# Kernel optimization log

Measured on AMD Instinct MI355X. Metric: run time of the kernel, lower is better.

Reference implementation:

```python
import jax, jax.numpy as jnp
import numpy as np

# Fixed graph/model dims (see shape_source)
C = 16      # cardinality
SUB = 64    # representation_size // cardinality
R = 1024    # representation_size
E = 1024    # node_encoding_size
S = 1024    # processed spatial feature size
G = 256     # global (FPN) channels
NH = 64     # number of human nodes
N = 256     # total number of nodes (humans first)
P = NH * N  # number of (human, node) pairs
EPS = 1e-5


def _layernorm(x, g, b):
    mu = jnp.mean(x, axis=-1, keepdims=True)
    var = jnp.var(x, axis=-1, keepdims=True)
    return (x - mu) * jax.lax.rsqrt(var + EPS) * g + b


def _pair_head(app, spat, W1, b1, W2, b2, W3, b3):
    # app: [P_or_1, A], spat: [P, S] -> [P, R]  (sum over cardinality; NO outer relu)
    a1 = jnp.einsum('pi,cis->cps', app, W1) + b1[:, None, :]   # [C,P_or_1,SUB]
    a2 = jnp.einsum('pj,cjs->cps', spat, W2) + b2[:, None, :]  # [C,P,SUB]
    h = jax.nn.relu(a1 * a2)                                   # broadcast over P
    return jnp.einsum('cps,csr->pr', h, W3) + jnp.sum(b3, axis=0)


def reference(node_encodings, spatial_raw, global_feat,
              sp_W1, sp_b1, sp_W2, sp_b2, sp_W3, sp_b3,
              ah_W1, ah_b1, ah_W2, ah_b2, ah_W3, ah_b3,
              o2s_W1, o2s_b1, o2s_W2, o2s_b2, o2s_W3, o2s_b3,
              s2o_W1, s2o_b1, s2o_W2, s2o_b2, s2o_W3, s2o_b3,
              ahg_W1, ahg_b1, ahg_W2, ahg_b2, ahg_W3, ahg_b3,
              adj_W, adj_b, lnh_g, lnh_b, lno_g, lno_b):
    # spatial head MLP: 36 -> 128 -> 256 -> 1024 with ReLU
    sp = jax.nn.relu(spatial_raw @ sp_W1 + sp_b1)
    sp = jax.nn.relu(sp @ sp_W2 + sp_b2)
    sp = jax.nn.relu(sp @ sp_W3 + sp_b3)            # [P, S]
    sp3 = sp.reshape(NH, N, S)                      # [NH, N, S]

    x_idx = jnp.repeat(jnp.arange(NH), N)           # [P]
    y_idx = jnp.tile(jnp.arange(N), NH)             # [P]

    h_enc = node_encodings[:NH]                     # humans are permuted to the top
    o_enc = node_encodings

    for _ in range(1):  # num_iter
        app_pairs = jnp.concatenate([h_enc[x_idx], o_enc[y_idx]], axis=1)  # [P, 2E]
        weights = jax.nn.relu(_pair_head(app_pairs, sp, ah_W1, ah_b1, ah_W2, ah_b2, ah_W3, ah_b3))
        adj = (weights @ adj_W + adj_b).reshape(NH, N)

        # obj_to_sub (node_type='object'): appearance = all node encodings
        a1 = jnp.einsum('ni,cis->cns', o_enc, o2s_W1) + o2s_b1[:, None, :]          # [C,N,SUB]
        a2 = jnp.einsum('hnj,cjs->chns', sp3, o2s_W2) + o2s_b2[:, None, None, :]    # [C,NH,N,SUB]
        m = jnp.einsum('chns,csr->hnr', jax.nn.relu(a1[:, None] * a2), o2s_W3) + jnp.sum(o2s_b3, axis=0)
        msg_h = jax.nn.relu(jnp.sum(jax.nn.softmax(adj, axis=1)[..., None] * m, axis=1))  # [NH,R]
        h_enc = _layernorm(h_enc + msg_h, lnh_g, lnh_b)

        # sub_to_obj (node_type='human'): appearance = human encodings
        a1 = jnp.einsum('hi,cis->chs', h_enc, s2o_W1) + s2o_b1[:, None, :]          # [C,NH,SUB]
        a2 = jnp.einsum('hnj,cjs->cnhs', sp3, s2o_W2) + s2o_b2[:, None, None, :]    # [C,N,NH,SUB]
        m = jnp.einsum('cnhs,csr->nhr', jax.nn.relu(a1[:, None] * a2), s2o_W3) + jnp.sum(s2o_b3, axis=0)
        msg_o = jax.nn.relu(jnp.sum(jax.nn.softmax(adj.T, axis=1)[..., None] * m, axis=1))  # [N,R]
        o_enc = _layernorm(o_enc + msg_o, lno_g, lno_b)

    app_final = jnp.concatenate([h_enc[x_idx], o_enc[y_idx]], axis=1)               # [P, 2E]
    f_local = jax.nn.relu(_pair_head(app_final, sp, ah_W1, ah_b1, ah_W2, ah_b2, ah_W3, ah_b3))
    f_glob = jax.nn.relu(_pair_head(global_feat, sp, ahg_W1, ahg_b1, ahg_W2, ahg_b2, ahg_W3, ahg_b3))
    return jnp.concatenate([f_local, f_glob], axis=1)  # [P, 2R]


def setup_inputs() -> dict:
    key = jax.random.key(0)
    ks = iter(jax.random.split(key, 64))
    def rn(shape, scale=0.05):
        return jax.random.normal(next(ks), shape, dtype=jnp.float32) * scale
    inp = {
        'node_encodings': jax.random.normal(next(ks), (N, E), dtype=jnp.float32),
        'spatial_raw': jax.random.normal(next(ks), (P, 36), dtype=jnp.float32),
        'global_feat': jax.random.normal(next(ks), (1, G), dtype=jnp.float32),
        'sp_W1': rn((36, 128)), 'sp_b1': jnp.zeros(128, jnp.float32),
        'sp_W2': rn((128, 256)), 'sp_b2': jnp.zeros(256, jnp.float32),
        'sp_W3': rn((256, S)), 'sp_b3': jnp.zeros(S, jnp.float32),
        'ah_W1': rn((C, 2 * E, SUB)), 'ah_b1': jnp.zeros((C, SUB), jnp.float32),
        'ah_W2': rn((C, S, SUB)), 'ah_b2': jnp.zeros((C, SUB), jnp.float32),
        'ah_W3': rn((C, SUB, R)), 'ah_b3': jnp.zeros((C, R), jnp.float32),
        'o2s_W1': rn((C, E, SUB)), 'o2s_b1': jnp.zeros((C, SUB), jnp.float32),
        'o2s_W2': rn((C, S, SUB)), 'o2s_b2': jnp.zeros((C, SUB), jnp.float32),
        'o2s_W3': rn((C, SUB, R)), 'o2s_b3': jnp.zeros((C, R), jnp.float32),
        's2o_W1': rn((C, E, SUB)), 's2o_b1': jnp.zeros((C, SUB), jnp.float32),
        's2o_W2': rn((C, S, SUB)), 's2o_b2': jnp.zeros((C, SUB), jnp.float32),
        's2o_W3': rn((C, SUB, R)), 's2o_b3': jnp.zeros((C, R), jnp.float32),
        'ahg_W1': rn((C, G, SUB)), 'ahg_b1': jnp.zeros((C, SUB), jnp.float32),
        'ahg_W2': rn((C, S, SUB)), 'ahg_b2': jnp.zeros((C, SUB), jnp.float32),
        'ahg_W3': rn((C, SUB, R)), 'ahg_b3': jnp.zeros((C, R), jnp.float32),
        'adj_W': rn((R, 1)), 'adj_b': jnp.zeros(1, jnp.float32),
        'lnh_g': jnp.ones(E, jnp.float32), 'lnh_b': jnp.zeros(E, jnp.float32),
        'lno_g': jnp.ones(E, jnp.float32), 'lno_b': jnp.zeros(E, jnp.float32),
    }
    return inp
```

## Files before the change

### kernel.cpp

```cpp
#include <hip/hip_runtime.h>
#include <hip/hip_bf16.h>
#include <stdint.h>
#include <stddef.h>

using bf16 = __hip_bfloat16;
typedef __bf16 bf16x8 __attribute__((ext_vector_type(8)));
typedef float f32x4 __attribute__((ext_vector_type(4)));

#define P_  16384

__device__ __forceinline__ void gload16(const void* g, void* l) {
    __builtin_amdgcn_global_load_lds((const __attribute__((address_space(1))) void*)g,
                                     (__attribute__((address_space(3))) void*)l, 16, 0, 0);
}

struct GArgs {
    const bf16* A; const bf16* B; void* C;
    const float* bias;
    const float* aux1;
    int M, N, K, ldc, kchunk;
    void* dst1; void* dst2; void* dst3; void* dstH;
    const float* cb0; const float* cb1; const float* cb2; const float* cb3;
    const float* a1gv; const float* Ahp; const float* Aop; const float* b1p;
};

template<int MODE, bool RELU, bool BIAS>
__global__ __launch_bounds__(256, 4)
void gemm_bt(GArgs g)
{
    __shared__ __align__(16) bf16 As[128 * 64];
    __shared__ __align__(16) bf16 Bs[128 * 64];

    const int tid  = threadIdx.x;
    const int wave = tid >> 6;
    const int lane = tid & 63;
    const int tileM = blockIdx.x * 128;
    const int tileN = blockIdx.y * 128;
    const int wr = (wave >> 1) << 6;
    const int wc = (wave & 1) << 6;
    const int M = g.M, N = g.N, K = g.K;

    const bf16* Ap = g.A; const bf16* Bp = g.B;
    void* Cp = g.C; const float* biasp = g.bias;
    if (MODE == 0 && blockIdx.z == 1) {
        Ap = (const bf16*)g.dst1; Bp = (const bf16*)g.dst2;
        Cp = g.dst3; biasp = g.cb1;
    }

    f32x4 acc[4][4] = {};

    const int gk = (((lane & 7) ^ (lane >> 3)) << 3);
    int arow[4], brow[4];
    #pragma unroll
    for (int j = 0; j < 4; ++j) {
        int r = wave * 32 + j * 8 + (lane >> 3);
        int gr = tileM + r; if (gr > M - 1) gr = M - 1; arow[j] = gr;
        int gn = tileN + r; if (gn > N - 1) gn = N - 1; brow[j] = gn;
    }
    const int m0 = wr + (lane & 15);
    const int n0 = wc + (lane & 15);
    const int q  = lane >> 4;

    int kbeg = 0, kend = K;
    if constexpr (MODE == 2) { kbeg = blockIdx.z * 64; kend = kbeg + 64; }

    for (int k0 = kbeg; k0 < kend; k0 += 64) {
        #pragma unroll
        for (int j = 0; j < 4; ++j) {
            int c = wave * 256 + j * 64 + lane;
            gload16(Ap + (size_t)arow[j] * K + k0 + gk, (void*)(As + c * 8));
            gload16(Bp + (size_t)brow[j] * K + k0 + gk, (void*)(Bs + c * 8));
        }
        __syncthreads();
        #pragma unroll
        for (int kk = 0; kk < 2; ++kk) {
            const int gs = ((kk << 2) + q) ^ (lane & 7);
            bf16x8 af[4], bfv[4];
            #pragma unroll
            for (int i = 0; i < 4; ++i) {
                af[i]  = *(const bf16x8*)(As + (m0 + i * 16) * 64 + gs * 8);
                bfv[i] = *(const bf16x8*)(Bs + (n0 + i * 16) * 64 + gs * 8);
            }
            #pragma unroll
            for (int i = 0; i < 4; ++i)
                #pragma unroll
                for (int j = 0; j < 4; ++j)
                    acc[i][j] = __builtin_amdgcn_mfma_f32_16x16x32_bf16(af[i], bfv[j], acc[i][j], 0, 0, 0);
        }
        __syncthreads();
    }

    const int rbase = tileM + wr + ((lane >> 4) << 2);
    const int cbase = tileN + wc + (lane & 15);

    if constexpr (MODE == 0 || MODE == 1) {
        #pragma unroll
        for (int i = 0; i < 4; ++i)
            #pragma unroll
            for (int j = 0; j < 4; ++j)
                #pragma unroll
                for (int r = 0; r < 4; ++r) {
                    int grow = rbase + i * 16 + r;
                    if (grow >= M) continue;
                    int gcol = cbase + j * 16;
                    float v = acc[i][j][r];
                    if (BIAS) v += biasp[gcol];
                    if (RELU) v = fmaxf(v, 0.f);
                    if (MODE == 1) ((bf16*)Cp)[(size_t)grow * g.ldc + gcol] = __float2bfloat16(v);
                    else           ((float*)Cp)[(size_t)grow * g.ldc + gcol] = v;
                }
    } else if constexpr (MODE == 2) {
        #pragma unroll
        for (int i = 0; i < 4; ++i)
            #pragma unroll
            for (int j = 0; j < 4; ++j)
                #pragma unroll
                for (int r = 0; r < 4; ++r) {
                    int grow = rbase + i * 16 + r;
                    if (grow >= M) continue;
                    atomicAdd((float*)Cp + (size_t)grow * g.ldc + cbase + j * 16, acc[i][j][r]);
                }
    } else if constexpr (MODE == 6) {
        #pragma unroll
        for (int i = 0; i < 4; ++i)
            #pragma unroll
            for (int r = 0; r < 4; ++r) {
                float s = 0.f;
                #pragma unroll
                for (int j = 0; j < 4; ++j) {
                    int gcol = cbase + j * 16;
                    s += fmaxf(acc[i][j][r] + biasp[gcol], 0.f) * g.aux1[gcol];
                }
                s += __shfl_xor(s, 1); s += __shfl_xor(s, 2);
                s += __shfl_xor(s, 4); s += __shfl_xor(s, 8);
                if ((lane & 15) == 0)
                    atomicAdd((float*)Cp + rbase + i * 16 + r, s);
            }
    } else if constexpr (MODE == 9) {
        int grp = tileN >> 10;
        int lcb = (tileN & 1023) + wc + (lane & 15);
        #pragma unroll
        for (int i = 0; i < 4; ++i)
            #pragma unroll
            for (int j = 0; j < 4; ++j)
                #pragma unroll
                for (int r = 0; r < 4; ++r) {
                    int p    = rbase + i * 16 + r;
                    int lcol = lcb + j * 16;
                    float accv = acc[i][j][r];
                    if (grp == 0) {
                        bf16 a2b = __float2bfloat16(accv + g.cb0[lcol]);
                        ((bf16*)Cp)[(size_t)p * 1024 + lcol] = a2b;
                        float a1 = g.Ahp[((size_t)(p >> 8)) * 3072 + lcol]
                                 + g.Aop[((size_t)(p & 255)) * 3072 + lcol] + g.b1p[lcol];
                        ((bf16*)g.dstH)[(size_t)p * 1024 + lcol] =
                            __float2bfloat16(fmaxf(a1 * (float)a2b, 0.f));
                    } else if (grp == 1) {
                        ((bf16*)g.dst1)[(size_t)p * 1024 + lcol] =
                            __float2bfloat16(accv + g.cb1[lcol]);
                    } else if (grp == 2) {
                        ((bf16*)g.dst2)[(size_t)p * 1024 + lcol] =
                            __float2bfloat16(accv + g.cb2[lcol]);
                    } else {
                        float a2v = accv + g.cb3[lcol];
                        ((bf16*)g.dst3)[(size_t)p * 1024 + lcol] =
                            __float2bfloat16(fmaxf(g.a1gv[lcol] * a2v, 0.f));
                    }
                }
    }
}

static GArgs mkargs(const bf16* A, const bf16* B, void* C, const float* bias,
                    const float* aux1, int M, int N, int K, int ldc, int kchunk)
{
    GArgs g{};
    g.A = A; g.B = B; g.C = C; g.bias = bias; g.aux1 = aux1;
    g.M = M; g.N = N; g.K = K; g.ldc = ldc; g.kchunk = kchunk;
    return g;
}

__global__ void reduce_o2s(const bf16* __restrict__ a2, const float* __restrict__ a1,
                           const float* __restrict__ b1, const float* __restrict__ sh,
                           bf16* __restrict__ out)
{
    int h = blockIdx.y, cq = blockIdx.x;
    int ng = threadIdx.x >> 5, ct = threadIdx.x & 31;
    int c = cq * 256 + ct * 8;
    float b1v[8], accv[8] = {};
    #pragma unroll
    for (int j = 0; j < 8; ++j) b1v[j] = b1[c + j];
    const float* shh = sh + h * 256;
    for (int n = ng; n < 256; n += 8) {
        float w = shh[n];
        bf16x8 a2v = *(const bf16x8*)(a2 + ((size_t)(h * 256 + n) << 10) + c);
        const float* a1p = a1 + (size_t)n * 3072 + c;
        #pragma unroll
        for (int j = 0; j < 8; ++j)
            accv[j] += w * fmaxf((a1p[j] + b1v[j]) * (float)a2v[j], 0.f);
    }
    __shared__ float red[8][264];
    #pragma unroll
    for (int j = 0; j < 8; ++j) red[ng][ct * 8 + j] = accv[j];
    __syncthreads();
    for (int s = 4; s > 0; s >>= 1) {
        if (ng < s)
            #pragma unroll
            for (int j = 0; j < 8; ++j) red[ng][ct * 8 + j] += red[ng + s][ct * 8 + j];
        __syncthreads();
    }
    if (ng == 0) {
        bf16x8 o;
        #pragma unroll
        for (int j = 0; j < 8; ++j) o[j] = (__bf16)red[0][ct * 8 + j];
        *(bf16x8*)(out + (size_t)h * 1024 + c) = o;
    }
}

__global__ void reduce_s2o(const bf16* __restrict__ a2, const float* __restrict__ a1,
                           const float* __restrict__ b1, const float* __restrict__ so,
                           bf16* __restrict__ out)
{
    int n = blockIdx.y, cq = blockIdx.x;
    int hg = threadIdx.x >> 5, ct = threadIdx.x & 31;
    int c = cq * 256 + ct * 8;
    float b1v[8], accv[8] = {};
    #pragma unroll
    for (int j = 0; j < 8; ++j) b1v[j] = b1[c + j];
    const float* son = so + n * 64;
    #pragma unroll
    for (int hh = 0; hh < 8; ++hh) {
        int h = hg + hh * 8;
        float w = son[h];
        bf16x8 a2v = *(const bf16x8*)(a2 + ((size_t)(h * 256 + n) << 10) + c);
        const float* a1p = a1 + (size_t)h * 2048 + c;
        #pragma unroll
        for (int j = 0; j < 8; ++j)
            accv[j] += w * fmaxf((a1p[j] + b1v[j]) * (float)a2v[j], 0.f);
    }
    __shared__ float red[8][264];
    #pragma unroll
    for (int j = 0; j < 8; ++j) red[hg][ct * 8 + j] = accv[j];
    __syncthreads();
    for (int s = 4; s > 0; s >>= 1) {
        if (hg < s)
            #pragma unroll
            for (int j = 0; j < 8; ++j) red[hg][ct * 8 + j] += red[hg + s][ct * 8 + j];
        __syncthreads();
    }
    if (hg == 0) {
        bf16x8 o;
        #pragma unroll
        for (int j = 0; j < 8; ++j) o[j] = (__bf16)red[0][ct * 8 + j];
        *(bf16x8*)(out + (size_t)n * 1024 + c) = o;
    }
}

__global__ void transp(const float* __restrict__ src, bf16* __restrict__ dst,
                       int rows, int cols, size_t sstride, size_t dstride)
{
    const float* s = src + blockIdx.z * sstride;
    bf16*        d = dst + blockIdx.z * dstride;
    __shared__ float tile[32][33];
    int c0 = blockIdx.x * 32, r0 = blockIdx.y * 32;
    int x = threadIdx.x, y = threadIdx.y;
    for (int yy = y; yy < 32; yy += 8) {
        int r = r0 + yy, c = c0 + x;
        tile[yy][x] = (r < rows && c < cols) ? s[(size_t)r * cols + c] : 0.f;
    }
    __syncthreads();
    for (int yy = y; yy < 32; yy += 8) {
        int c = c0 + yy, r = r0 + x;
        if (c < cols && r < rows) d[(size_t)c * rows + r] = __float2bfloat16(tile[x][yy]);
    }
}

struct T9 { const float* s[9]; bf16* d[9]; size_t ss[9]; };
__global__ void transp64b(T9 t)
{
    int pair = blockIdx.z >> 4, slice = blockIdx.z & 15;
    const float* s = t.s[pair] + slice * t.ss[pair];
    bf16*        d = t.d[pair] + slice * 65536;
    __shared__ float tile[32][33];
    int c0 = blockIdx.x * 32, r0 = blockIdx.y * 32;
    int x = threadIdx.x, y = threadIdx.y;
    for (int yy = y; yy < 32; yy += 8)
        tile[yy][x] = s[(size_t)(r0 + yy) * 64 + c0 + x];
    __syncthreads();
    for (int yy = y; yy < 32; yy += 8)
        d[(size_t)(c0 + yy) * 1024 + r0 + x] = __float2bfloat16(tile[x][yy]);
}

struct T4 { const float* s[4]; bf16* d[4]; };
__global__ void transp1024b(T4 t)
{
    const float* s = t.s[blockIdx.z];
    bf16*        d = t.d[blockIdx.z];
    __shared__ float tile[32][33];
    int c0 = blockIdx.x * 32, r0 = blockIdx.y * 32;
    int x = threadIdx.x, y = threadIdx.y;
    for (int yy = y; yy < 32; yy += 8)
        tile[yy][x] = s[(size_t)(r0 + yy) * 1024 + c0 + x];
    __syncthreads();
    for (int yy = y; yy < 32; yy += 8)
        d[(size_t)(c0 + yy) * 1024 + r0 + x] = __float2bfloat16(tile[x][yy]);
}

__global__ void conv_spw1(const float* __restrict__ src, bf16* __restrict__ dst) {
    int i = blockIdx.x * 256 + threadIdx.x;
    if (i >= 128 * 64) return;
    int k = i & 63, n = i >> 6;
    dst[i] = __float2bfloat16(k < 36 ? src[k * 128 + n] : 0.f);
}

__global__ void pad_spatial(const float* __restrict__ src, bf16* __restrict__ dst) {
    int i = blockIdx.x * 256 + threadIdx.x;
    int k = i & 63, p = i >> 6;
    dst[i] = __float2bfloat16(k < 36 ? src[p * 36 + k] : 0.f);
}

__global__ void cast_f2b(const float* __restrict__ src, bf16* __restrict__ dst, int n) {
    int i = blockIdx.x * 256 + threadIdx.x;
    if (i < n) dst[i] = __float2bfloat16(src[i]);
}

struct S4 { const float* s[4]; float* d[4]; };
__global__ void sumb3b(S4 a) {
    int i = blockIdx.x * 256 + threadIdx.x;
    int pair = i >> 10, r = i & 1023;
    const float* b3 = a.s[pair];
    float s = 0.f;
    #pragma unroll
    for (int c = 0; c < 16; ++c) s += b3[c * 1024 + r];
    a.d[pair][r] = s;
}

__global__ void hbuild(const float* __restrict__ Ah, int ah_ld,
                       const float* __restrict__ Ao, int ao_ld,
                       const float* __restrict__ b1, const bf16* __restrict__ a2,
                       bf16* __restrict__ H)
{
    size_t base = ((size_t)blockIdx.x * 256 + threadIdx.x) * 8;
    int cs = (int)(base & 1023);
    int p  = (int)(base >> 10);
    const float* ph = Ah + (size_t)(p >> 8) * ah_ld + cs;
    const float* po = Ao + (size_t)(p & 255) * ao_ld + cs;
    bf16x8 av = *(const bf16x8*)(a2 + base);
    bf16x8 o;
    #pragma unroll
    for (int j = 0; j < 8; ++j) {
        float a1 = ph[j] + po[j] + b1[cs + j];
        o[j] = (__bf16)fmaxf(a1 * (float)av[j], 0.f);
    }
    *(bf16x8*)(H + base) = o;
}

__global__ void softmax_h(const float* __restrict__ adj, float* __restrict__ sh) {
    int h = blockIdx.x, n = threadIdx.x;
    __shared__ float red[256];
    float v = adj[h * 256 + n];
    red[n] = v; __syncthreads();
    for (int s = 128; s > 0; s >>= 1) { if (n < s) red[n] = fmaxf(red[n], red[n + s]); __syncthreads(); }
    float m = red[0]; __syncthreads();
    float e = expf(v - m);
    red[n] = e; __syncthreads();
    for (int s = 128; s > 0; s >>= 1) { if (n < s) red[n] += red[n + s]; __syncthreads(); }
    sh[h * 256 + n] = e / red[0];
}

__global__ void softmax_o(const float* __restrict__ adj, float* __restrict__ so) {
    int n = blockIdx.x, h = threadIdx.x;
    float v = adj[h * 256 + n];
    float m = v;
    #pragma unroll
    for (int off = 32; off; off >>= 1) m = fmaxf(m, __shfl_xor(m, off));
    float e = expf(v - m);
    float s = e;
    #pragma unroll
    for (int off = 32; off; off >>= 1) s += __shfl_xor(s, off);
    so[n * 64 + h] = e / s;
}

__global__ void ln_k(const float* __restrict__ x, const float* __restrict__ msgraw,
                     const float* __restrict__ sb3,
                     const float* __restrict__ g, const float* __restrict__ bb,
                     bf16* __restrict__ out)
{
    int row = blockIdx.x, t = threadIdx.x;
    const float* xr = x + (size_t)row * 1024;
    const float* mr = msgraw + (size_t)row * 1024;
    float v[4]; float s = 0.f, ss = 0.f;
    #pragma unroll
    for (int j = 0; j < 4; ++j) {
        int i = t + j * 256;
        v[j] = xr[i] + fmaxf(mr[i] + sb3[i], 0.f);
        s += v[j]; ss += v[j] * v[j];
    }
    __shared__ float r1[256], r2[256];
    r1[t] = s; r2[t] = ss; __syncthreads();
    for (int k = 128; k > 0; k >>= 1) { if (t < k) { r1[t] += r1[t + k]; r2[t] += r2[t + k]; } __syncthreads(); }
    float mean = r1[0] * (1.f / 1024.f);
    float var  = r2[0] * (1.f / 1024.f) - mean * mean;
    float inv  = rsqrtf(var + 1e-5f);
    #pragma unroll
    for (int j = 0; j < 4; ++j) {
        int i = t + j * 256;
        out[(size_t)row * 1024 + i] = __float2bfloat16((v[j] - mean) * inv * g[i] + bb[i]);
    }
}

__global__ void a1g_k(const float* __restrict__ gf, const float* __restrict__ W1,
                      const float* __restrict__ b1, float* __restrict__ a1g)
{
    int cs = blockIdx.x * 256 + threadIdx.x;
    int c = cs >> 6, s = cs & 63;
    float acc = b1[cs];
    for (int g = 0; g < 256; ++g) acc += gf[g] * W1[((size_t)c * 256 + g) * 64 + s];
    a1g[cs] = acc;
}

extern "C" void kernel_launch(void* const* d_in, const int* in_sizes, int n_in,
                              void* d_out, int out_size, void* d_ws, size_t ws_size,
                              hipStream_t stream)
{
    const float* node_enc = (const float*)d_in[0];
    const float* spatial  = (const float*)d_in[1];
    const float* gfeat    = (const float*)d_in[2];
    const float* sp_W1 = (const float*)d_in[3];  const float* sp_b1 = (const float*)d_in[4];
    const float* sp_W2 = (const float*)d_in[5];  const float* sp_b2 = (const float*)d_in[6];
    const float* sp_W3 = (const float*)d_in[7];  const float* sp_b3 = (const float*)d_in[8];
    const float* ah_W1 = (const float*)d_in[9];  const float* ah_b1 = (const float*)d_in[10];
    const float* ah_W2 = (const float*)d_in[11]; const float* ah_b2 = (const float*)d_in[12];
    const float* ah_W3 = (const float*)d_in[13]; const float* ah_b3 = (const float*)d_in[14];
    const float* o2s_W1 = (const float*)d_in[15]; const float* o2s_b1 = (const float*)d_in[16];
    const float* o2s_W2 = (const float*)d_in[17]; const float* o2s_b2 = (const float*)d_in[18];
    const float* o2s_W3 = (const float*)d_in[19]; const float* o2s_b3 = (const float*)d_in[20];
    const float* s2o_W1 = (const float*)d_in[21]; const float* s2o_b1 = (const float*)d_in[22];
    const float* s2o_W2 = (const float*)d_in[23]; const float* s2o_b2 = (const float*)d_in[24];
    const float* s2o_W3 = (const float*)d_in[25]; const float* s2o_b3 = (const float*)d_in[26];
    const float* ahg_W1 = (const float*)d_in[27]; const float* ahg_b1 = (const float*)d_in[28];
    const float* ahg_W2 = (const float*)d_in[29]; const float* ahg_b2 = (const float*)d_in[30];
    const float* ahg_W3 = (const float*)d_in[31]; const float* ahg_b3 = (const float*)d_in[32];
    const float* adj_W = (const float*)d_in[33];
    const float* lnh_g = (const float*)d_in[35]; const float* lnh_b = (const float*)d_in[36];
    const float* lno_g = (const float*)d_in[37]; const float* lno_b = (const float*)d_in[38];

    char* w = (char*)d_ws;
    auto alloc = [&](size_t bytes) { char* p = w; w += (bytes + 255) & ~(size_t)255; return p; };
    bf16*  sp      = (bf16*)alloc((size_t)P_ * 1024 * 2);
    bf16*  a2_ah   = (bf16*)alloc((size_t)P_ * 1024 * 2);
    bf16*  Hbuf    = (bf16*)alloc((size_t)P_ * 1024 * 2);
    bf16*  a2_o2s  = (bf16*)alloc((size_t)P_ * 1024 * 2);
    bf16*  a2_s2o  = (bf16*)alloc((size_t)P_ * 1024 * 2);
    bf16*  H_ahg   = (bf16*)alloc((size_t)P_ * 1024 * 2);
    bf16*  spat_pad= (bf16*)alloc((size_t)P_ * 64 * 2);
    bf16*  spL1    = (bf16*)alloc((size_t)P_ * 128 * 2);
    bf16*  spL2    = (bf16*)alloc((size_t)P_ * 256 * 2);
    bf16*  enc_bf  = (bf16*)alloc(256 * 1024 * 2);
    bf16*  henc_bf = (bf16*)alloc(64 * 1024 * 2);
    bf16*  oenc_bf = (bf16*)alloc(256 * 1024 * 2);
    bf16*  HredH   = (bf16*)alloc(64 * 1024 * 2);
    bf16*  HredO   = (bf16*)alloc(256 * 1024 * 2);
    bf16*  spW1t   = (bf16*)alloc(128 * 64 * 2);
    bf16*  spW2t   = (bf16*)alloc(256 * 128 * 2);
    bf16*  spW3t   = (bf16*)alloc(1024 * 256 * 2);
    bf16*  W2cat   = (bf16*)alloc((size_t)4096 * 1024 * 2);
    bf16*  W1cat3  = (bf16*)alloc((size_t)3072 * 1024 * 2);
    bf16*  W1catF  = (bf16*)alloc((size_t)2048 * 1024 * 2);
    bf16*  ahW3t   = (bf16*)alloc(1024 * 1024 * 2);
    bf16*  o2sW3t  = (bf16*)alloc(1024 * 1024 * 2);
    bf16*  s2oW3t  = (bf16*)alloc(1024 * 1024 * 2);
    bf16*  ahgW3t  = (bf16*)alloc(1024 * 1024 * 2);
    float* Aoa1x = (float*)alloc(256 * 3072 * 4);
    float* A1f   = (float*)alloc(64 * 2048 * 4);
    float* Ao_f  = (float*)alloc(256 * 1024 * 4);
    size_t z1_bytes = (size_t)(256 * 3072 + 64 * 2048 + 256 * 1024) * 4 + 1024;
    float* adjv  = (float*)alloc(P_ * 4);
    float* msgh  = (float*)alloc(64 * 1024 * 4);
    float* msgo  = (float*)alloc(256 * 1024 * 4);
    size_t z2_bytes = (size_t)(P_ + 64 * 1024 + 256 * 1024) * 4 + 1024;
    float* sh    = (float*)alloc(P_ * 4);
    float* so    = (float*)alloc(P_ * 4);
    float* a1g   = (float*)alloc(1024 * 4);
    float* sb3_ah  = (float*)alloc(4096);
    float* sb3_o2s = (float*)alloc(4096);
    float* sb3_s2o = (float*)alloc(4096);
    float* sb3_ahg = (float*)alloc(4096);

    hipMemsetAsync(Aoa1x, 0, z1_bytes, stream);
    hipMemsetAsync(adjv,  0, z2_bytes, stream);

    {
        T9 t;
        t.s[0] = ah_W1;                     t.d[0] = W1cat3 + (size_t)2048 * 1024; t.ss[0] = (size_t)2048 * 64;
        t.s[1] = ah_W1 + (size_t)1024 * 64; t.d[1] = W1cat3;                       t.ss[1] = (size_t)2048 * 64;
        t.s[2] = o2s_W1;                    t.d[2] = W1cat3 + (size_t)1024 * 1024; t.ss[2] = 65536;
        t.s[3] = s2o_W1;                    t.d[3] = W1catF;                       t.ss[3] = 65536;
        t.s[4] = ah_W1;                     t.d[4] = W1catF + (size_t)1024 * 1024; t.ss[4] = (size_t)2048 * 64;
        t.s[5] = ah_W2;                     t.d[5] = W2cat;                        t.ss[5] = 65536;
        t.s[6] = o2s_W2;                    t.d[6] = W2cat + (size_t)1024 * 1024;  t.ss[6] = 65536;
        t.s[7] = s2o_W2;                    t.d[7] = W2cat + (size_t)2048 * 1024;  t.ss[7] = 65536;
        t.s[8] = ahg_W2;                    t.d[8] = W2cat + (size_t)3072 * 1024;  t.ss[8] = 65536;
        transp64b<<<dim3(2, 32, 144), dim3(32, 8), 0, stream>>>(t);
    }
    {
        T4 t;
        t.s[0] = ah_W3;  t.d[0] = ahW3t;
        t.s[1] = o2s_W3; t.d[1] = o2sW3t;
        t.s[2] = s2o_W3; t.d[2] = s2oW3t;
        t.s[3] = ahg_W3; t.d[3] = ahgW3t;
        transp1024b<<<dim3(32, 32, 4), dim3(32, 8), 0, stream>>>(t);
    }
    dim3 tb(32, 8);
    conv_spw1<<<32, 256, 0, stream>>>(sp_W1, spW1t);
    transp<<<dim3(8, 4, 1),  tb, 0, stream>>>(sp_W2, spW2t, 128, 256, 0, 0);
    transp<<<dim3(32, 8, 1), tb, 0, stream>>>(sp_W3, spW3t, 256, 1024, 0, 0);
    pad_spatial<<<4096, 256, 0, stream>>>(spatial, spat_pad);
    cast_f2b<<<1024, 256, 0, stream>>>(node_enc, enc_bf, 256 * 1024);
    {
        S4 a;
        a.s[0] = ah_b3;  a.d[0] = sb3_ah;
        a.s[1] = o2s_b3; a.d[1] = sb3_o2s;
        a.s[2] = s2o_b3; a.d[2] = sb3_s2o;
        a.s[3] = ahg_b3; a.d[3] = sb3_ahg;
        sumb3b<<<16, 256, 0, stream>>>(a);
    }
    a1g_k<<<4, 256, 0, stream>>>(gfeat, ahg_W1, ahg_b1, a1g);

    gemm_bt<2, false, false><<<dim3(2, 24, 16), 256, 0, stream>>>(
        mkargs(enc_bf, W1cat3, Aoa1x, nullptr, nullptr, 256, 3072, 1024, 3072, 64));

    gemm_bt<1, true, true><<<dim3(128, 1), 256, 0, stream>>>(
        mkargs(spat_pad, spW1t, spL1, sp_b1, nullptr, P_, 128, 64, 128, 0));
    gemm_bt<1, true, true><<<dim3(128, 2), 256, 0, stream>>>(
        mkargs(spL1, spW2t, spL2, sp_b2, nullptr, P_, 256, 128, 256, 0));
    gemm_bt<1, true, true><<<dim3(128, 8), 256, 0, stream>>>(
        mkargs(spL2, spW3t, sp, sp_b3, nullptr, P_, 1024, 256, 1024, 0));

    {
        GArgs g = mkargs(sp, W2cat, a2_ah, nullptr, nullptr, P_, 4096, 1024, 1024, 0);
        g.dst1 = a2_o2s; g.dst2 = a2_s2o; g.dst3 = H_ahg; g.dstH = Hbuf;
        g.cb0 = ah_b2; g.cb1 = o2s_b2; g.cb2 = s2o_b2; g.cb3 = ahg_b2;
        g.a1gv = a1g; g.Ahp = Aoa1x + 2048; g.Aop = Aoa1x; g.b1p = ah_b1;
        gemm_bt<9, false, false><<<dim3(128, 32), 256, 0, stream>>>(g);
    }

    gemm_bt<6, false, false><<<dim3(128, 8), 256, 0, stream>>>(
        mkargs(Hbuf, ahW3t, adjv, sb3_ah, adj_W, P_, 1024, 1024, 1024, 0));
    softmax_h<<<64, 256, 0, stream>>>(adjv, sh);
    softmax_o<<<256, 64, 0, stream>>>(adjv, so);

    reduce_o2s<<<dim3(4, 64), 256, 0, stream>>>(a2_o2s, Aoa1x + 1024, o2s_b1, sh, HredH);
    gemm_bt<2, false, false><<<dim3(1, 8, 16), 256, 0, stream>>>(
        mkargs(HredH, o2sW3t, msgh, nullptr, nullptr, 64, 1024, 1024, 1024, 64));
    ln_k<<<64, 256, 0, stream>>>(node_enc, msgh, sb3_o2s, lnh_g, lnh_b, henc_bf);

    gemm_bt<2, false, false><<<dim3(1, 16, 16), 256, 0, stream>>>(
        mkargs(henc_bf, W1catF, A1f, nullptr, nullptr, 64, 2048, 1024, 2048, 64));

    reduce_s2o<<<dim3(4, 256), 256, 0, stream>>>(a2_s2o, A1f, s2o_b1, so, HredO);
    gemm_bt<2, false, false><<<dim3(2, 8, 16), 256, 0, stream>>>(
        mkargs(HredO, s2oW3t, msgo, nullptr, nullptr, 256, 1024, 1024, 1024, 64));
    ln_k<<<256, 256, 0, stream>>>(node_enc, msgo, sb3_s2o, lno_g, lno_b, oenc_bf);

    gemm_bt<2, false, false><<<dim3(2, 8, 16), 256, 0, stream>>>(
        mkargs(oenc_bf, W1cat3, Ao_f, nullptr, nullptr, 256, 1024, 1024, 1024, 64));
    hbuild<<<8192, 256, 0, stream>>>(A1f + 1024, 2048, Ao_f, 1024, ah_b1, a2_ah, Hbuf);

    {
        GArgs g = mkargs(Hbuf, ahW3t, (float*)d_out, sb3_ah, nullptr, P_, 1024, 1024, 2048, 0);
        g.dst1 = (void*)H_ahg; g.dst2 = (void*)ahgW3t;
        g.dst3 = (void*)((float*)d_out + 1024); g.cb1 = sb3_ahg;
        gemm_bt<0, true, true><<<dim3(128, 8, 2), 256, 0, stream>>>(g);
    }

    (void)in_sizes; (void)n_in; (void)out_size; (void)ws_size;
}
```

Baseline: 798.2 us.

## Add 256x256 double-buffered GEMM kernel for large pair GEMMs

Introduces a new 512-thread GEMM with 256x256 tiles, double-buffered LDS staging via direct global-to-LDS loads, interleaved prefetch with MFMA phases, s_setprio, and XCD-aware block remapping. The large P-dimension GEMMs (spatial layer 3, the fused W2 projection, adjacency head, final output) move to it. The larger tiles are meant to raise arithmetic intensity and hide load latency, at the cost of more LDS use and registers, hence lower occupancy. The MODE 0 dual-problem dispatch moves from the old kernel to the new one.

After: 905.8 us. 13.5% more time.

```diff
diff --git a/kernel.cpp b/kernel.cpp
--- a/kernel.cpp
+++ b/kernel.cpp
@@ -42,10 +42,6 @@
 
     const bf16* Ap = g.A; const bf16* Bp = g.B;
     void* Cp = g.C; const float* biasp = g.bias;
-    if (MODE == 0 && blockIdx.z == 1) {
-        Ap = (const bf16*)g.dst1; Bp = (const bf16*)g.dst2;
-        Cp = g.dst3; biasp = g.cb1;
-    }
 
     f32x4 acc[4][4] = {};
 
@@ -120,9 +116,173 @@
                     if (grow >= M) continue;
                     atomicAdd((float*)Cp + (size_t)grow * g.ldc + cbase + j * 16, acc[i][j][r]);
                 }
+    }
+}
+
+template<int MODE, bool RELU, bool BIAS>
+__global__ __launch_bounds__(512, 2)
+void gemm256(GArgs g)
+{
+    __shared__ __align__(16) bf16 AS[2][256 * 64];
+    __shared__ __align__(16) bf16 BS[2][256 * 64];
+
+    const int tid  = threadIdx.x;
+    const int wave = tid >> 6;
+    const int lane = tid & 63;
+    const int wr = wave >> 2;
+    const int wc = wave & 3;
+    const int l15 = lane & 15, l7 = lane & 7, q = lane >> 4;
+
+    const int nx  = gridDim.x;
+    const int nwg = nx * gridDim.y;
+    int lin = blockIdx.y * nx + blockIdx.x;
+    if ((nwg & 7) == 0) lin = (lin & 7) * (nwg >> 3) + (lin >> 3);
+    const int tileM = (lin % nx) * 256;
+    const int tileN = (lin / nx) * 256;
+
+    const int K = g.K;
+
+    const bf16* Ap = g.A; const bf16* Bp = g.B;
+    void* Cp = g.C; const float* biasp = g.bias;
+    if (MODE == 0 && blockIdx.z == 1) {
+        Ap = (const bf16*)g.dst1; Bp = (const bf16*)g.dst2;
+        Cp = g.dst3; biasp = g.cb1;
+    }
+
+    const int srow = tid >> 3;
+    const int gk   = ((lane & 7) ^ (lane >> 3)) << 3;
+    const bf16* Ag = Ap + (size_t)(tileM + srow) * K + gk;
+    const bf16* Bg = Bp + (size_t)(tileN + srow) * K + gk;
+    const int t8 = tid * 8;
+
+    const int aoff = (wr * 128 + l15) * 64;
+    const int boff = (wc * 64  + l15) * 64;
+    const int s0 = ((q    ) ^ l7) << 3;
+    const int s1 = ((q + 4) ^ l7) << 3;
+
+    f32x4 acc[8][4] = {};
+    const int nkt = K >> 6;
+
+#define STAGE_A(bb, kt_, j_) gload16(Ag + (size_t)(j_) * 64 * K + (kt_) * 64, (void*)(&AS[bb][(j_) * 4096 + t8]))
+#define STAGE_B(bb, kt_, j_) gload16(Bg + (size_t)(j_) * 64 * K + (kt_) * 64, (void*)(&BS[bb][(j_) * 4096 + t8]))
+#define FENCE asm volatile("" ::: "memory")
+
+    STAGE_B(0, 0, 0); STAGE_B(0, 0, 1); STAGE_B(0, 0, 2); STAGE_B(0, 0, 3);
+    STAGE_A(0, 0, 0); STAGE_A(0, 0, 2); STAGE_A(0, 0, 1); STAGE_A(0, 0, 3);
+    asm volatile("s_waitcnt vmcnt(2)" ::: "memory");
+    __builtin_amdgcn_s_barrier();
+    FENCE;
+
+    for (int kt = 0; kt < nkt; ++kt) {
+        const int b = kt & 1;
+        const bf16* As_ = AS[b];
+        const bf16* Bs_ = BS[b];
+        const bool pf = (kt + 1 < nkt);
+        bf16x8 af[4][2], bfv[4][2];
+
+        #pragma unroll
+        for (int i = 0; i < 4; ++i) {
+            af[i][0] = *(const bf16x8*)(As_ + aoff + i * 1024 + s0);
+            af[i][1] = *(const bf16x8*)(As_ + aoff + i * 1024 + s1);
+        }
+        #pragma unroll
+        for (int j = 0; j < 2; ++j) {
+            bfv[j][0] = *(const bf16x8*)(Bs_ + boff + j * 1024 + s0);
+            bfv[j][1] = *(const bf16x8*)(Bs_ + boff + j * 1024 + s1);
+        }
+        if (pf) { STAGE_B(b ^ 1, kt + 1, 0); STAGE_B(b ^ 1, kt + 1, 1); }
+        FENCE; __builtin_amdgcn_s_barrier();
+        asm volatile("s_waitcnt lgkmcnt(0)" ::: "memory");
+        __builtin_amdgcn_s_setprio(1);
+        #pragma unroll
+        for (int i = 0; i < 4; ++i)
+            #pragma unroll
+            for (int j = 0; j < 2; ++j)
+                #pragma unroll
+                for (int kk = 0; kk < 2; ++kk)
+                    acc[i][j] = __builtin_amdgcn_mfma_f32_16x16x32_bf16(af[i][kk], bfv[j][kk], acc[i][j], 0, 0, 0);
+        __builtin_amdgcn_s_setprio(0);
+        FENCE; __builtin_amdgcn_s_barrier();
+
+        #pragma unroll
+        for (int j = 2; j < 4; ++j) {
+            bfv[j][0] = *(const bf16x8*)(Bs_ + boff + j * 1024 + s0);
+            bfv[j][1] = *(const bf16x8*)(Bs_ + boff + j * 1024 + s1);
+        }
+        if (pf) { STAGE_B(b ^ 1, kt + 1, 2); STAGE_B(b ^ 1, kt + 1, 3); }
+        FENCE; __builtin_amdgcn_s_barrier();
+        asm volatile("s_waitcnt lgkmcnt(0)" ::: "memory");
+        __builtin_amdgcn_s_setprio(1);
+        #pragma unroll
+        for (int i = 0; i < 4; ++i)
+            #pragma unroll
+            for (int j = 2; j < 4; ++j)
+                #pragma unroll
+                for (int kk = 0; kk < 2; ++kk)
+                    acc[i][j] = __builtin_amdgcn_mfma_f32_16x16x32_bf16(af[i][kk], bfv[j][kk], acc[i][j], 0, 0, 0);
+        __builtin_amdgcn_s_setprio(0);
+        if (pf) asm volatile("s_waitcnt vmcnt(4)" ::: "memory");
+        else    asm volatile("s_waitcnt vmcnt(0)" ::: "memory");
+        FENCE; __builtin_amdgcn_s_barrier();
+
+        #pragma unroll
+        for (int i = 0; i < 4; ++i) {
+            af[i][0] = *(const bf16x8*)(As_ + aoff + 4096 + i * 1024 + s0);
+            af[i][1] = *(const bf16x8*)(As_ + aoff + 4096 + i * 1024 + s1);
+        }
+        if (pf) { STAGE_A(b ^ 1, kt + 1, 0); STAGE_A(b ^ 1, kt + 1, 2); }
+        FENCE; __builtin_amdgcn_s_barrier();
+        asm volatile("s_waitcnt lgkmcnt(0)" ::: "memory");
+        __builtin_amdgcn_s_setprio(1);
+        #pragma unroll
+        for (int i = 0; i < 4; ++i)
+            #pragma unroll
+            for (int j = 0; j < 2; ++j)
+                #pragma unroll
+                for (int kk = 0; kk < 2; ++kk)
+                    acc[4 + i][j] = __builtin_amdgcn_mfma_f32_16x16x32_bf16(af[i][kk], bfv[j][kk], acc[4 + i][j], 0, 0, 0);
+        __builtin_amdgcn_s_setprio(0);
+        FENCE; __builtin_amdgcn_s_barrier();
+
+        if (pf) { STAGE_A(b ^ 1, kt + 1, 1); STAGE_A(b ^ 1, kt + 1, 3); }
+        FENCE; __builtin_amdgcn_s_barrier();
+        __builtin_amdgcn_s_setprio(1);
+        #pragma unroll
+        for (int i = 0; i < 4; ++i)
+            #pragma unroll
+            for (int j = 2; j < 4; ++j)
+                #pragma unroll
+                for (int kk = 0; kk < 2; ++kk)
+                    acc[4 + i][j] = __builtin_amdgcn_mfma_f32_16x16x32_bf16(af[i][kk], bfv[j][kk], acc[4 + i][j], 0, 0, 0);
+        __builtin_amdgcn_s_setprio(0);
+        asm volatile("s_waitcnt vmcnt(2)" ::: "memory");
+        FENCE; __builtin_amdgcn_s_barrier();
+    }
+#undef STAGE_A
+#undef STAGE_B
+#undef FENCE
+
+    const int rbase = tileM + wr * 128 + (q << 2);
+    const int cbase = tileN + wc * 64 + l15;
+
+    if constexpr (MODE == 0 || MODE == 1) {
+        #pragma unroll
+        for (int i = 0; i < 8; ++i)
+            #pragma unroll
+            for (int j = 0; j < 4; ++j)
+                #pragma unroll
+                for (int r = 0; r < 4; ++r) {
+                    int grow = rbase + i * 16 + r;
+                    int gcol = cbase + j * 16;
+                    float v = acc[i][j][r];
+                    if (BIAS) v += biasp[gcol];
+                    if (RELU) v = fmaxf(v, 0.f);
+                    if (MODE == 1) ((bf16*)Cp)[(size_t)grow * g.ldc + gcol] = __float2bfloat16(v);
+                    else           ((float*)Cp)[(size_t)grow * g.ldc + gcol] = v;
+                }
     } else if constexpr (MODE == 6) {
         #pragma unroll
-        for (int i = 0; i < 4; ++i)
+        for (int i = 0; i < 8; ++i)
             #pragma unroll
             for (int r = 0; r < 4; ++r) {
                 float s = 0.f;
@@ -133,14 +293,14 @@
                 }
                 s += __shfl_xor(s, 1); s += __shfl_xor(s, 2);
                 s += __shfl_xor(s, 4); s += __shfl_xor(s, 8);
-                if ((lane & 15) == 0)
+                if (l15 == 0)
                     atomicAdd((float*)Cp + rbase + i * 16 + r, s);
             }
     } else if constexpr (MODE == 9) {
-        int grp = tileN >> 10;
-        int lcb = (tileN & 1023) + wc + (lane & 15);
-        #pragma unroll
-        for (int i = 0; i < 4; ++i)
+        const int grp = tileN >> 10;
+        const int lcb = (tileN & 1023) + wc * 64 + l15;
+        #pragma unroll
+        for (int i = 0; i < 8; ++i)
             #pragma unroll
             for (int j = 0; j < 4; ++j)
                 #pragma unroll
@@ -533,7 +693,7 @@
         mkargs(spat_pad, spW1t, spL1, sp_b1, nullptr, P_, 128, 64, 128, 0));
     gemm_bt<1, true, true><<<dim3(128, 2), 256, 0, stream>>>(
         mkargs(spL1, spW2t, spL2, sp_b2, nullptr, P_, 256, 128, 256, 0));
-    gemm_bt<1, true, true><<<dim3(128, 8), 256, 0, stream>>>(
+    gemm256<1, true, true><<<dim3(64, 4), 512, 0, stream>>>(
         mkargs(spL2, spW3t, sp, sp_b3, nullptr, P_, 1024, 256, 1024, 0));
 
     {
@@ -541,10 +701,10 @@
         g.dst1 = a2_o2s; g.dst2 = a2_s2o; g.dst3 = H_ahg; g.dstH = Hbuf;
         g.cb0 = ah_b2; g.cb1 = o2s_b2; g.cb2 = s2o_b2; g.cb3 = ahg_b2;
         g.a1gv = a1g; g.Ahp = Aoa1x + 2048; g.Aop = Aoa1x; g.b1p = ah_b1;
-        gemm_bt<9, false, false><<<dim3(128, 32), 256, 0, stream>>>(g);
-    }
-
-    gemm_bt<6, false, false><<<dim3(128, 8), 256, 0, stream>>>(
+        gemm256<9, false, false><<<dim3(64, 16), 512, 0, stream>>>(g);
+    }
+
+    gemm256<6, false, false><<<dim3(64, 4), 512, 0, stream>>>(
         mkargs(Hbuf, ahW3t, adjv, sb3_ah, adj_W, P_, 1024, 1024, 1024, 0));
     softmax_h<<<64, 256, 0, stream>>>(adjv, sh);
     softmax_o<<<256, 64, 0, stream>>>(adjv, so);
@@ -570,7 +730,7 @@
         GArgs g = mkargs(Hbuf, ahW3t, (float*)d_out, sb3_ah, nullptr, P_, 1024, 1024, 2048, 0);
         g.dst1 = (void*)H_ahg; g.dst2 = (void*)ahgW3t;
         g.dst3 = (void*)((float*)d_out + 1024); g.cb1 = sb3_ahg;
-        gemm_bt<0, true, true><<<dim3(128, 8, 2), 256, 0, stream>>>(g);
+        gemm256<0, true, true><<<dim3(64, 4, 2), 512, 0, stream>>>(g);
     }
 
     (void)in_sizes; (void)n_in; (void)out_size; (void)ws_size;
```

## Add 256x256 double-buffered 8-wave GEMM kernel for the large pair GEMMs

Applied to the files above, without the earlier changes.

Introduces a new GEMM kernel with 256x256 tiles, 512 threads, double-buffered LDS, interleaved global-to-LDS loads with MFMA phases, s_setprio, and an XCD-aware block remap. It replaces the 128x128 kernel for the big P-row GEMMs (spatial layer 3, the fused W2 GEMM, the adjacency GEMM and the final output GEMM). The goal is more data reuse per block and overlap of loads with math to raise MFMA throughput. It uses a lot of LDS (128KB) and registers and drops M/N bounds clamping, so it assumes tile-divisible shapes.

Result: slower. 917.7 us (+15.0%).

```diff
diff --git a/kernel.cpp b/kernel.cpp
--- a/kernel.cpp
+++ b/kernel.cpp
@@ -42,10 +42,6 @@
 
     const bf16* Ap = g.A; const bf16* Bp = g.B;
     void* Cp = g.C; const float* biasp = g.bias;
-    if (MODE == 0 && blockIdx.z == 1) {
-        Ap = (const bf16*)g.dst1; Bp = (const bf16*)g.dst2;
-        Cp = g.dst3; biasp = g.cb1;
-    }
 
     f32x4 acc[4][4] = {};
 
@@ -120,9 +116,166 @@
                     if (grow >= M) continue;
                     atomicAdd((float*)Cp + (size_t)grow * g.ldc + cbase + j * 16, acc[i][j][r]);
                 }
+    }
+}
+
+template<int MODE, bool RELU, bool BIAS>
+__global__ __launch_bounds__(512, 2)
+void gemm256(GArgs g)
+{
+    __shared__ __align__(16) bf16 AS0[256 * 64];
+    __shared__ __align__(16) bf16 AS1[256 * 64];
+    __shared__ __align__(16) bf16 BS0[256 * 64];
+    __shared__ __align__(16) bf16 BS1[256 * 64];
+
+    const int tid  = threadIdx.x;
+    const int wave = tid >> 6;
+    const int lane = tid & 63;
+    const int wr = wave >> 2;
+    const int wc = wave & 3;
+    const int l15 = lane & 15, l7 = lane & 7, q = lane >> 4;
+
+    const int nx  = gridDim.x;
+    const int nwg = nx * gridDim.y;
+    int lin = blockIdx.y * nx + blockIdx.x;
+    if ((nwg & 7) == 0) lin = (lin & 7) * (nwg >> 3) + (lin >> 3);
+    const int tileM = (lin % nx) * 256;
+    const int tileN = (lin / nx) * 256;
+
+    const int K = g.K;
+
+    const bf16* Ap = g.A; const bf16* Bp = g.B;
+    void* Cp = g.C; const float* biasp = g.bias;
+    if (MODE == 0 && blockIdx.z == 1) {
+        Ap = (const bf16*)g.dst1; Bp = (const bf16*)g.dst2;
+        Cp = g.dst3; biasp = g.cb1;
+    }
+
+    const int srow = tid >> 3;
+    const int gk   = ((lane & 7) ^ (lane >> 3)) << 3;
+    const bf16* Ag = Ap + (size_t)(tileM + srow) * K + gk;
+    const bf16* Bg = Bp + (size_t)(tileN + srow) * K + gk;
+    const int t8 = tid * 8;
+
+    const int aoff = (wr * 128 + l15) * 64;
+    const int boff = (wc * 64  + l15) * 64;
+    const int s0 = ((q    ) ^ l7) << 3;
+    const int s1 = ((q + 4) ^ l7) << 3;
+
+    f32x4 acc[8][4] = {};
+    const int nkt = K >> 6;
+
+#define SA(AD, kt_, j_) gload16(Ag + (size_t)(j_) * 64 * K + (size_t)(kt_) * 64, (void*)((AD) + (j_) * 4096 + t8))
+#define SB(BD, kt_, j_) gload16(Bg + (size_t)(j_) * 64 * K + (size_t)(kt_) * 64, (void*)((BD) + (j_) * 4096 + t8))
+
+#define MM4x2(IB, BF, JB) \
+    _Pragma("unroll") for (int i_ = 0; i_ < 4; ++i_) \
+    _Pragma("unroll") for (int j_ = 0; j_ < 2; ++j_) \
+    _Pragma("unroll") for (int kk_ = 0; kk_ < 2; ++kk_) \
+        acc[(IB) + i_][(JB) + j_] = __builtin_amdgcn_mfma_f32_16x16x32_bf16(af[i_][kk_], BF[j_][kk_], acc[(IB) + i_][(JB) + j_], 0, 0, 0);
+
+#define TILE(RD_A, RD_B, WR_A, WR_B, kt) do {                                          \
+    const bf16* As_ = (RD_A); const bf16* Bs_ = (RD_B);                                \
+    bf16x8 af[4][2], bfv[2][2], bfw[2][2];                                             \
+             \
+    _Pragma("unroll") for (int i_ = 0; i_ < 4; ++i_) {                                 \
+        af[i_][0] = *(const bf16x8*)(As_ + aoff + i_ * 1024 + s0);                     \
+        af[i_][1] = *(const bf16x8*)(As_ + aoff + i_ * 1024 + s1);                     \
+    }                                                                                  \
+    _Pragma("unroll") for (int j_ = 0; j_ < 2; ++j_) {                                 \
+        bfv[j_][0] = *(const bf16x8*)(Bs_ + boff + j_ * 1024 + s0);                    \
+        bfv[j_][1] = *(const bf16x8*)(Bs_ + boff + j_ * 1024 + s1);                    \
+    }                                                                                  \
+    SA(WR_A, (kt) + 1, 0); SA(WR_A, (kt) + 1, 2);                                      \
+    asm volatile("s_waitcnt lgkmcnt(8)");                                              \
+    __builtin_amdgcn_s_barrier();                                                      \
+    asm volatile("s_waitcnt lgkmcnt(0)");                                              \
+    __builtin_amdgcn_s_setprio(1);                                                     \
+    MM4x2(0, bfv, 0);                                                                  \
+    __builtin_amdgcn_s_setprio(0);                                                     \
+    __builtin_amdgcn_s_barrier();                                                      \
+                   \
+    _Pragma("unroll") for (int j_ = 0; j_ < 2; ++j_) {                                 \
+        bfw[j_][0] = *(const bf16x8*)(Bs_ + boff + (2 + j_) * 1024 + s0);              \
+        bfw[j_][1] = *(const bf16x8*)(Bs_ + boff + (2 + j_) * 1024 + s1);              \
+    }                                                                                  \
+    SB(WR_B, (kt) + 1, 0); SB(WR_B, (kt) + 1, 1);                                      \
+    __builtin_amdgcn_s_barrier();                                                      \
+    asm volatile("s_waitcnt lgkmcnt(0)");                                              \
+    __builtin_amdgcn_s_setprio(1);                                                     \
+    MM4x2(0, bfw, 2);                                                                  \
+    __builtin_amdgcn_s_setprio(0);                                                     \
+    asm volatile("s_waitcnt vmcnt(4)" ::: "memory");                                   \
+    __builtin_amdgcn_s_barrier();                                                      \
+                    \
+    _Pragma("unroll") for (int i_ = 0; i_ < 4; ++i_) {                                 \
+        af[i_][0] = *(const bf16x8*)(As_ + aoff + 4096 + i_ * 1024 + s0);              \
+        af[i_][1] = *(const bf16x8*)(As_ + aoff + 4096 + i_ * 1024 + s1);              \
+    }                                                                                  \
+    SB(WR_B, (kt) + 1, 2); SB(WR_B, (kt) + 1, 3);                                      \
+    __builtin_amdgcn_s_barrier();                                                      \
+    asm volatile("s_waitcnt lgkmcnt(0)");                                              \
+    __builtin_amdgcn_s_setprio(1);                                                     \
+    MM4x2(4, bfw, 2);                                                                  \
+    __builtin_amdgcn_s_setprio(0);                                                     \
+    __builtin_amdgcn_s_barrier();                                                      \
+         \
+    _Pragma("unroll") for (int j_ = 0; j_ < 2; ++j_) {                                 \
+        bfv[j_][0] = *(const bf16x8*)(Bs_ + boff + j_ * 1024 + s0);                    \
+        bfv[j_][1] = *(const bf16x8*)(Bs_ + boff + j_ * 1024 + s1);                    \
+    }                                                                                  \
+    SA(WR_A, (kt) + 1, 1); SA(WR_A, (kt) + 1, 3);                                      \
+    __builtin_amdgcn_s_barrier();                                                      \
+    asm volatile("s_waitcnt lgkmcnt(0)");                                              \
+    __builtin_amdgcn_s_setprio(1);                                                     \
+    MM4x2(4, bfv, 0);                                                                  \
+    __builtin_amdgcn_s_setprio(0);                                                     \
+    asm volatile("s_waitcnt vmcnt(2)" ::: "memory");                                   \
+    __builtin_amdgcn_s_barrier();                                                      \
+    asm volatile("" ::: "memory");                                                     \
+} while (0)
+
+    SA(AS0, 0, 0); SA(AS0, 0, 2);
+    SB(BS0, 0, 0); SB(BS0, 0, 1); SB(BS0, 0, 2); SB(BS0, 0, 3);
+    SA(AS0, 0, 1); SA(AS0, 0, 3);
+    asm volatile("s_waitcnt vmcnt(2)" ::: "memory");
+    __builtin_amdgcn_s_barrier();
+    asm volatile("" ::: "memory");
+
+    const int niter = nkt >> 1;
+    for (int it = 0; it < niter; ++it) {
+        const int kt0 = it * 2;
+        TILE(AS0, BS0, AS1, BS1, kt0);
+        TILE(AS1, BS1, AS0, BS0, kt0 + 1);
+    }
+    asm volatile("s_waitcnt vmcnt(0)" ::: "memory");
+
+#undef TILE
+#undef MM4x2
+#undef SA
+#undef SB
+
+    const int rbase = tileM + wr * 128 + (q << 2);
+    const int cbase = tileN + wc * 64 + l15;
+
+    if constexpr (MODE == 0 || MODE == 1) {
+        #pragma unroll
+        for (int i = 0; i < 8; ++i)
+            #pragma unroll
+            for (int j = 0; j < 4; ++j)
+                #pragma unroll
+                for (int r = 0; r < 4; ++r) {
+                    int grow = rbase + i * 16 + r;
+                    int gcol = cbase + j * 16;
+                    float v = acc[i][j][r];
+                    if (BIAS) v += biasp[gcol];
+                    if (RELU) v = fmaxf(v, 0.f);
+                    if (MODE == 1) ((bf16*)Cp)[(size_t)grow * g.ldc + gcol] = __float2bfloat16(v);
+                    else           ((float*)Cp)[(size_t)grow * g.ldc + gcol] = v;
+                }
     } else if constexpr (MODE == 6) {
         #pragma unroll
-        for (int i = 0; i < 4; ++i)
+        for (int i = 0; i < 8; ++i)
             #pragma unroll
             for (int r = 0; r < 4; ++r) {
                 float s = 0.f;
@@ -133,14 +286,14 @@
                 }
                 s += __shfl_xor(s, 1); s += __shfl_xor(s, 2);
                 s += __shfl_xor(s, 4); s += __shfl_xor(s, 8);
-                if ((lane & 15) == 0)
+                if (l15 == 0)
                     atomicAdd((float*)Cp + rbase + i * 16 + r, s);
             }
     } else if constexpr (MODE == 9) {
-        int grp = tileN >> 10;
-        int lcb = (tileN & 1023) + wc + (lane & 15);
-        #pragma unroll
-        for (int i = 0; i < 4; ++i)
+        const int grp = tileN >> 10;
+        const int lcb = (tileN & 1023) + wc * 64 + l15;
+        #pragma unroll
+        for (int i = 0; i < 8; ++i)
             #pragma unroll
             for (int j = 0; j < 4; ++j)
                 #pragma unroll
@@ -485,6 +638,7 @@
     float* sb3_o2s = (float*)alloc(4096);
     float* sb3_s2o = (float*)alloc(4096);
     float* sb3_ahg = (float*)alloc(4096);
+    (void)alloc(65536);
 
     hipMemsetAsync(Aoa1x, 0, z1_bytes, stream);
     hipMemsetAsync(adjv,  0, z2_bytes, stream);
@@ -533,7 +687,7 @@
         mkargs(spat_pad, spW1t, spL1, sp_b1, nullptr, P_, 128, 64, 128, 0));
     gemm_bt<1, true, true><<<dim3(128, 2), 256, 0, stream>>>(
         mkargs(spL1, spW2t, spL2, sp_b2, nullptr, P_, 256, 128, 256, 0));
-    gemm_bt<1, true, true><<<dim3(128, 8), 256, 0, stream>>>(
+    gemm256<1, true, true><<<dim3(64, 4), 512, 0, stream>>>(
         mkargs(spL2, spW3t, sp, sp_b3, nullptr, P_, 1024, 256, 1024, 0));
 
     {
@@ -541,10 +695,10 @@
         g.dst1 = a2_o2s; g.dst2 = a2_s2o; g.dst3 = H_ahg; g.dstH = Hbuf;
         g.cb0 = ah_b2; g.cb1 = o2s_b2; g.cb2 = s2o_b2; g.cb3 = ahg_b2;
         g.a1gv = a1g; g.Ahp = Aoa1x + 2048; g.Aop = Aoa1x; g.b1p = ah_b1;
-        gemm_bt<9, false, false><<<dim3(128, 32), 256, 0, stream>>>(g);
-    }
-
-    gemm_bt<6, false, false><<<dim3(128, 8), 256, 0, stream>>>(
+        gemm256<9, false, false><<<dim3(64, 16), 512, 0, stream>>>(g);
+    }
+
+    gemm256<6, false, false><<<dim3(64, 4), 512, 0, stream>>>(
         mkargs(Hbuf, ahW3t, adjv, sb3_ah, adj_W, P_, 1024, 1024, 1024, 0));
     softmax_h<<<64, 256, 0, stream>>>(adjv, sh);
     softmax_o<<<256, 64, 0, stream>>>(adjv, so);
@@ -570,7 +724,7 @@
         GArgs g = mkargs(Hbuf, ahW3t, (float*)d_out, sb3_ah, nullptr, P_, 1024, 1024, 2048, 0);
         g.dst1 = (void*)H_ahg; g.dst2 = (void*)ahgW3t;
         g.dst3 = (void*)((float*)d_out + 1024); g.cb1 = sb3_ahg;
-        gemm_bt<0, true, true><<<dim3(128, 8, 2), 256, 0, stream>>>(g);
+        gemm256<0, true, true><<<dim3(64, 4, 2), 512, 0, stream>>>(g);
     }
 
     (void)in_sizes; (void)n_in; (void)out_size; (void)ws_size;
```
